# Kernel optimization log

Measured on AMD Instinct MI355X. Metric: run time of the kernel, lower is better.

## Reference

```python
import jax, jax.numpy as jnp
import numpy as np

N_HEADS = 12
EPS = 1e-6
H_DIM = 768


def setup_inputs() -> dict:
    key = jax.random.key(0)
    ks = jax.random.split(key, 10)
    B, M, T, C = 2, 64, 512, H_DIM
    x = jax.random.normal(ks[0], (B, M, T, C), dtype=jnp.float32)
    mask = jnp.ones((B, M, T), dtype=jnp.float32)
    s = 1.0 / np.sqrt(C)
    Wq = jax.random.normal(ks[1], (C, C), dtype=jnp.float32) * s
    bq = jax.random.normal(ks[2], (C,), dtype=jnp.float32) * 0.01
    Wk = jax.random.normal(ks[3], (C, C), dtype=jnp.float32) * s
    bk = jax.random.normal(ks[4], (C,), dtype=jnp.float32) * 0.01
    Wv = jax.random.normal(ks[5], (C, C), dtype=jnp.float32) * s
    bv = jax.random.normal(ks[6], (C,), dtype=jnp.float32) * 0.01
    Wp = jax.random.normal(ks[7], (C, C), dtype=jnp.float32) * s
    bp = jax.random.normal(ks[8], (C,), dtype=jnp.float32) * 0.01
    return {"x": x, "mask": mask, "Wq": Wq, "bq": bq, "Wk": Wk, "bk": bk,
            "Wv": Wv, "bv": bv, "Wp": Wp, "bp": bp}


def reference(x, mask, Wq, bq, Wk, bk, Wv, bv, Wp, bp):
    B, M, T, C = x.shape
    N, D = N_HEADS, C // N_HEADS
    # projections: nn.Linear -> x @ W.T + b, then [B,M,T,N,D] -> [B,M,N,T,D]
    q = (x @ Wq.T + bq).reshape(B, M, T, N, D).transpose(0, 1, 3, 2, 4)
    k = (x @ Wk.T + bk).reshape(B, M, T, N, D).transpose(0, 1, 3, 2, 4)
    v = (x @ Wv.T + bv).reshape(B, M, T, N, D).transpose(0, 1, 3, 2, 4)
    q = jax.nn.elu(q) + 1.0
    k = jax.nn.elu(k) + 1.0
    k = k * mask[:, :, None, :, None]
    # KtV[b,m,n,d,e] = sum_t k[b,m,n,t,d] * v[b,m,n,t,e]   (small [D,D] per head)
    KtV = jnp.einsum('bmntd,bmnte->bmnde', k, v)
    # Z[b,m,n,t] = 1 / (q . sum_t' k + eps)
    Z = 1.0 / (jnp.einsum('bmntd,bmnd->bmnt', q, k.sum(axis=-2)) + EPS)
    # torch code does Z.expand(...,T,D) @ KtV, which equals Z * KtV.sum(over d)
    S = KtV.sum(axis=-2)                       # [B,M,N,E]
    V = Z[..., None] * S[:, :, :, None, :]     # [B,M,N,T,E]
    V = V.transpose(0, 1, 3, 2, 4).reshape(B, M, T, N * D)
    out = V @ Wp.T + bp
    return out
```

## Files before the change

kernel.cpp:

```cpp
#include <hip/hip_runtime.h>
#include <hip/hip_bf16.h>
#include <stdint.h>

typedef short short8 __attribute__((ext_vector_type(8)));
typedef float f32x4 __attribute__((ext_vector_type(4)));

#define EPS_Z 1e-6f

__device__ __forceinline__ unsigned short f2bf(float f) {
  uint32_t b = __float_as_uint(f);
  b += 0x7FFFu + ((b >> 16) & 1u);
  return (unsigned short)(b >> 16);
}
__device__ __forceinline__ float bf2f(unsigned short u) {
  return __uint_as_float(((uint32_t)u) << 16);
}

__device__ __forceinline__ void gl16(const unsigned short* g, unsigned short* l) {
  __builtin_amdgcn_global_load_lds(
      (const __attribute__((address_space(1))) unsigned int*)g,
      (__attribute__((address_space(3))) unsigned int*)l, 16, 0, 0);
}

__global__ __launch_bounds__(256) void k_cvt(const float* __restrict__ in,
                                             unsigned short* __restrict__ out, int n) {
  int i = (blockIdx.x * 256 + threadIdx.x) * 8;
  if (i >= n) return;
  float4 a = *(const float4*)(in + i);
  float4 b = *(const float4*)(in + i + 4);
  union { unsigned short u[8]; short8 v; } r;
  r.u[0] = f2bf(a.x); r.u[1] = f2bf(a.y); r.u[2] = f2bf(a.z); r.u[3] = f2bf(a.w);
  r.u[4] = f2bf(b.x); r.u[5] = f2bf(b.y); r.u[6] = f2bf(b.z); r.u[7] = f2bf(b.w);
  *(short8*)(out + i) = r.v;
}

__global__ __launch_bounds__(512, 2) void k_projqk(
    const unsigned short* __restrict__ xbf,
    const unsigned short* __restrict__ Wkbf,
    const unsigned short* __restrict__ Wqbf,
    const float* __restrict__ bk,
    const float* __restrict__ bq,
    const float* __restrict__ mask,
    float* __restrict__ kd,
    float* __restrict__ ksum_part,
    unsigned short* __restrict__ qbf)
{
  __shared__ unsigned short Ab[128][64];
  __shared__ unsigned short Bkb[128][64];
  __shared__ unsigned short Bqb[128][64];
  __shared__ float rowf[128];
  __shared__ float kcol[2][128];

  const int tid = threadIdx.x;
  const int lane = tid & 63;
  const int wid = tid >> 6;
  const int isQ = wid >> 2;
  const int w2 = wid & 3;
  const int wr = w2 >> 1, wc = w2 & 1;
  const int colTile = blockIdx.x;
  const int rowTile = blockIdx.y;
  const int bm = rowTile >> 2;
  const int trow = rowTile & 3;
  const size_t rowBase = (size_t)rowTile * 128;
  const int colBase = colTile * 128;
  const int lrow = lane & 15;
  const int lgrp = lane >> 4;

  if (tid < 128) rowf[tid] = mask[bm * 512 + trow * 128 + tid];

  f32x4 acc[4][4] = {};

  for (int kt = 0; kt < 12; ++kt) {
    const int k0 = kt * 64;
    __syncthreads();
#pragma unroll
    for (int c = 0; c < 2; ++c) {
      const int chunk = c * 512 + tid;
      const int r = chunk >> 3;
      const int cc = chunk & 7;
      const int scc = cc ^ (r & 7);
      const int ldst = c * 4096 + wid * 512;
      gl16(xbf + (rowBase + r) * 768 + k0 + scc * 8, &Ab[0][0] + ldst);
      gl16(Wkbf + (size_t)(colBase + r) * 768 + k0 + scc * 8, &Bkb[0][0] + ldst);
      gl16(Wqbf + (size_t)(colBase + r) * 768 + k0 + scc * 8, &Bqb[0][0] + ldst);
    }
    __syncthreads();
    const unsigned short* Bsel = isQ ? &Bqb[0][0] : &Bkb[0][0];
#pragma unroll
    for (int kk = 0; kk < 64; kk += 32) {
      short8 av[4], bv4[4];
#pragma unroll
      for (int rf = 0; rf < 4; ++rf) {
        const int row = wr * 64 + rf * 16 + lrow;
        const int cidx = ((kk >> 3) + lgrp) ^ (row & 7);
        av[rf] = *(const short8*)&Ab[row][cidx * 8];
      }
#pragma unroll
      for (int cf = 0; cf < 4; ++cf) {
        const int row = wc * 64 + cf * 16 + lrow;
        const int cidx = ((kk >> 3) + lgrp) ^ (row & 7);
        bv4[cf] = *(const short8*)(Bsel + row * 64 + cidx * 8);
      }
#pragma unroll
      for (int rf = 0; rf < 4; ++rf)
#pragma unroll
        for (int cf = 0; cf < 4; ++cf)
          acc[rf][cf] = __builtin_amdgcn_mfma_f32_16x16x32_bf16(
              av[rf], bv4[cf], acc[rf][cf], 0, 0, 0);
    }
  }

  const float* bias = isQ ? bq : bk;
  float bvv[4];
#pragma unroll
  for (int cf = 0; cf < 4; ++cf)
    bvv[cf] = bias[colBase + wc * 64 + cf * 16 + lrow];
#pragma unroll
  for (int rf = 0; rf < 4; ++rf)
#pragma unroll
    for (int cf = 0; cf < 4; ++cf)
#pragma unroll
      for (int j = 0; j < 4; ++j) {
        float v = acc[rf][cf][j] + bvv[cf];
        v = (v > 0.0f) ? (v + 1.0f) : __expf(v);
        if (!isQ) v *= rowf[wr * 64 + rf * 16 + lgrp * 4 + j];
        acc[rf][cf][j] = v;
      }

  const int head = colTile * 2 + wc;

  if (!isQ) {
#pragma unroll
    for (int rf = 0; rf < 4; ++rf)
#pragma unroll
      for (int j = 0; j < 4; ++j) {
        float s = acc[rf][0][j] + acc[rf][1][j] + acc[rf][2][j] + acc[rf][3][j];
        s += __shfl_xor(s, 1, 64);
        s += __shfl_xor(s, 2, 64);
        s += __shfl_xor(s, 4, 64);
        s += __shfl_xor(s, 8, 64);
        if ((lane & 15) == 0) {
          const int t = trow * 128 + wr * 64 + rf * 16 + lgrp * 4 + j;
          kd[((size_t)bm * 512 + t) * 12 + head] = s;
        }
      }
#pragma unroll
    for (int cf = 0; cf < 4; ++cf) {
      float s = 0.f;
#pragma unroll
      for (int rf = 0; rf < 4; ++rf)
#pragma unroll
        for (int j = 0; j < 4; ++j) s += acc[rf][cf][j];
      s += __shfl_xor(s, 16, 64);
      s += __shfl_xor(s, 32, 64);
      if (lane < 16) kcol[wr][wc * 64 + cf * 16 + lane] = s;
    }
  } else {
#pragma unroll
    for (int rf = 0; rf < 4; ++rf)
#pragma unroll
      for (int j = 0; j < 4; ++j) {
        const int t = trow * 128 + wr * 64 + rf * 16 + lgrp * 4 + j;
        unsigned short* qp = qbf + (((size_t)bm * 12 + head) * 512 + t) * 64 + lrow;
#pragma unroll
        for (int cf = 0; cf < 4; ++cf)
          qp[cf * 16] = f2bf(acc[rf][cf][j]);
      }
  }

  __syncthreads();
  if (tid < 128)
    ksum_part[((size_t)bm * 4 + trow) * 768 + colBase + tid] =
        kcol[0][tid] + kcol[1][tid];
}

__global__ __launch_bounds__(192) void k_xk(const unsigned short* __restrict__ xbf,
                                            const float* __restrict__ kd,
                                            float* __restrict__ xk_part) {
  __shared__ float kdl[128][12];
  const int bm = blockIdx.x, ts = blockIdx.y, tid = threadIdx.x;
  for (int i = tid; i < 128 * 12; i += 192)
    kdl[i / 12][i % 12] = kd[((size_t)bm * 512 + ts * 128 + i / 12) * 12 + (i % 12)];
  __syncthreads();
  float a[12][4];
#pragma unroll
  for (int n = 0; n < 12; ++n)
#pragma unroll
    for (int j = 0; j < 4; ++j) a[n][j] = 0.f;
  const int c = tid * 4;
  const unsigned short* xp = xbf + ((size_t)bm * 512 + ts * 128) * 768 + c;
  for (int t = 0; t < 128; ++t) {
    ushort4 xv = *(const ushort4*)(xp + (size_t)t * 768);
    const float x0 = bf2f(xv.x), x1 = bf2f(xv.y), x2 = bf2f(xv.z), x3 = bf2f(xv.w);
#pragma unroll
    for (int n = 0; n < 12; ++n) {
      const float kv = kdl[t][n];
      a[n][0] += kv * x0; a[n][1] += kv * x1; a[n][2] += kv * x2; a[n][3] += kv * x3;
    }
  }
  float* op = xk_part + ((size_t)bm * 4 + ts) * 12 * 768 + c;
#pragma unroll
  for (int n = 0; n < 12; ++n)
    *(float4*)(op + (size_t)n * 768) = make_float4(a[n][0], a[n][1], a[n][2], a[n][3]);
}

__global__ __launch_bounds__(256) void k_sg(const float* __restrict__ ksum_part,
                                            const float* __restrict__ xk_part,
                                            const float* __restrict__ Wv,
                                            const float* __restrict__ bv,
                                            const float* __restrict__ Wp,
                                            float* __restrict__ G) {
  __shared__ __align__(16) float xk_l[768];
  __shared__ __align__(16) float S_l[64];
  __shared__ float kdsum_s;
  const int bm = blockIdx.x, n = blockIdx.y, tid = threadIdx.x;

  if (tid < 192) {
    const float* xp = xk_part + (size_t)bm * 4 * 9216 + n * 768 + tid * 4;
    float4 a = *(const float4*)(xp);
    float4 b = *(const float4*)(xp + 9216);
    float4 c = *(const float4*)(xp + 18432);
    float4 d = *(const float4*)(xp + 27648);
    *(float4*)&xk_l[tid * 4] = make_float4(a.x + b.x + c.x + d.x,
                                           a.y + b.y + c.y + d.y,
                                           a.z + b.z + c.z + d.z,
                                           a.w + b.w + c.w + d.w);
  } else {
    const int d = tid - 192;
    const float* kp = ksum_part + (size_t)bm * 4 * 768 + n * 64 + d;
    float s = kp[0] + kp[768] + kp[1536] + kp[2304];
    s += __shfl_xor(s, 1, 64);
    s += __shfl_xor(s, 2, 64);
    s += __shfl_xor(s, 4, 64);
    s += __shfl_xor(s, 8, 64);
    s += __shfl_xor(s, 16, 64);
    s += __shfl_xor(s, 32, 64);
    if (d == 0) kdsum_s = s;
  }
  __syncthreads();

  {
    const int e = tid >> 2, q = tid & 3;
    const float4* wv = (const float4*)(Wv + (size_t)(n * 64 + e) * 768 + q * 192);
    const float4* xp4 = (const float4*)(xk_l + q * 192);
    float s = 0.f;
#pragma unroll
    for (int i = 0; i < 48; ++i) {
      float4 w = wv[i], xx = xp4[i];
      s += w.x * xx.x + w.y * xx.y + w.z * xx.z + w.w * xx.w;
    }
    s += __shfl_xor(s, 1, 64);
    s += __shfl_xor(s, 2, 64);
    if (q == 0) S_l[e] = s + bv[n * 64 + e] * kdsum_s;
  }
  __syncthreads();

#pragma unroll
  for (int r = 0; r < 3; ++r) {
    const int p = r * 256 + tid;
    const float4* wp = (const float4*)(Wp + (size_t)p * 768 + n * 64);
    const float4* sp = (const float4*)S_l;
    float g = 0.f;
#pragma unroll
    for (int i = 0; i < 16; ++i) {
      float4 w = wp[i], s = sp[i];
      g += w.x * s.x + w.y * s.y + w.z * s.z + w.w * s.w;
    }
    G[((size_t)bm * 12 + n) * 768 + p] = g;
  }
}

__global__ __launch_bounds__(256) void k_z(const unsigned short* __restrict__ qbf,
                                           const float* __restrict__ ksum_part,
                                           float* __restrict__ Z) {
  __shared__ float ksum_l[768];
  const int bm = blockIdx.x, ts = blockIdx.y, tid = threadIdx.x;
  for (int i = tid; i < 768; i += 256) {
    const float* kp = ksum_part + (size_t)bm * 3072 + i;
    ksum_l[i] = kp[0] + kp[768] + kp[1536] + kp[2304];
  }
  __syncthreads();
#pragma unroll
  for (int i = 0; i < 6; ++i) {
    const int task = i * 256 + tid;
    const int n = task >> 7;
    const int t = ts * 128 + (task & 127);
    const unsigned short* qp = qbf + (((size_t)bm * 12 + n) * 512 + t) * 64;
    const float* kp = &ksum_l[n * 64];
    float s = 0.f;
#pragma unroll
    for (int c = 0; c < 8; ++c) {
      short8 qv = *(const short8*)(qp + c * 8);
      s += bf2f((unsigned short)qv[0]) * kp[c * 8 + 0]
         + bf2f((unsigned short)qv[1]) * kp[c * 8 + 1]
         + bf2f((unsigned short)qv[2]) * kp[c * 8 + 2]
         + bf2f((unsigned short)qv[3]) * kp[c * 8 + 3]
         + bf2f((unsigned short)qv[4]) * kp[c * 8 + 4]
         + bf2f((unsigned short)qv[5]) * kp[c * 8 + 5]
         + bf2f((unsigned short)qv[6]) * kp[c * 8 + 6]
         + bf2f((unsigned short)qv[7]) * kp[c * 8 + 7];
    }
    Z[((size_t)bm * 12 + n) * 512 + t] = 1.0f / (s + EPS_Z);
  }
}

__global__ __launch_bounds__(256) void k_out(const float* __restrict__ Z,
                                             const float* __restrict__ G,
                                             const float* __restrict__ bp,
                                             float* __restrict__ outp) {
  __shared__ __align__(16) float G_l[9216];
  __shared__ float Z_l[768];
  __shared__ __align__(16) float bp_l[768];
  const int bm = blockIdx.x;
  const int tbase = blockIdx.y * 64;
  const int tid = threadIdx.x;
  for (int i = tid; i < 9216; i += 256) G_l[i] = G[(size_t)bm * 9216 + i];
  for (int i = tid; i < 768; i += 256) {
    bp_l[i] = bp[i];
    Z_l[i] = Z[((size_t)bm * 12 + (i >> 6)) * 512 + tbase + (i & 63)];
  }
  __syncthreads();
  for (int it = 0; it < 48; ++it) {
    const int idx = it * 1024 + tid * 4;
    const int t = idx / 768;
    const int p = idx - t * 768;
    float4 o = *(const float4*)&bp_l[p];
#pragma unroll
    for (int n = 0; n < 12; ++n) {
      const float z = Z_l[n * 64 + t];
      const float4 g = *(const float4*)&G_l[n * 768 + p];
      o.x += z * g.x; o.y += z * g.y; o.z += z * g.z; o.w += z * g.w;
    }
    *(float4*)&outp[((size_t)bm * 512 + tbase + t) * 768 + p] = o;
  }
}

extern "C" void kernel_launch(void* const* d_in, const int* in_sizes, int n_in,
                              void* d_out, int out_size, void* d_ws, size_t ws_size,
                              hipStream_t stream) {
  const float* x    = (const float*)d_in[0];
  const float* mask = (const float*)d_in[1];
  const float* Wq   = (const float*)d_in[2];
  const float* bq   = (const float*)d_in[3];
  const float* Wk   = (const float*)d_in[4];
  const float* bk   = (const float*)d_in[5];
  const float* Wv   = (const float*)d_in[6];
  const float* bv   = (const float*)d_in[7];
  const float* Wp   = (const float*)d_in[8];
  const float* bp   = (const float*)d_in[9];
  float* outp = (float*)d_out;

  char* ws = (char*)d_ws;
  unsigned short* xbf  = (unsigned short*)(ws);
  unsigned short* Wkbf = (unsigned short*)(ws + 100663296);
  unsigned short* Wqbf = (unsigned short*)(ws + 101842944);
  float* kd        = (float*)(ws + 103022592);
  float* ksum_part = (float*)(ws + 106168320);
  float* xk_part   = (float*)(ws + 107741184);
  float* Zb        = (float*)(ws + 126615552);
  float* G         = (float*)(ws + 129761280);
  unsigned short* qbf = (unsigned short*)d_out;

  hipLaunchKernelGGL(k_cvt, dim3(24576), dim3(256), 0, stream, x, xbf, 50331648);
  hipLaunchKernelGGL(k_cvt, dim3(288), dim3(256), 0, stream, Wk, Wkbf, 589824);
  hipLaunchKernelGGL(k_cvt, dim3(288), dim3(256), 0, stream, Wq, Wqbf, 589824);
  hipLaunchKernelGGL(k_projqk, dim3(6, 512), dim3(512), 0, stream,
                     xbf, Wkbf, Wqbf, bk, bq, mask, kd, ksum_part, qbf);
  hipLaunchKernelGGL(k_xk, dim3(128, 4), dim3(192), 0, stream, xbf, kd, xk_part);
  hipLaunchKernelGGL(k_sg, dim3(128, 12), dim3(256), 0, stream,
                     ksum_part, xk_part, Wv, bv, Wp, G);
  hipLaunchKernelGGL(k_z, dim3(128, 4), dim3(256), 0, stream, qbf, ksum_part, Zb);
  hipLaunchKernelGGL(k_out, dim3(128, 8), dim3(256), 0, stream, Zb, G, bp, outp);
}
```

Baseline: 494.2 us.

## Merge conversion launches, compute K and Q per wave, swizzle grid, fuse xk and Z kernels

The three bf16 conversion launches become one kernel, and the xk and Z kernels are merged into one launch that branches on block index. The QK projection now uses 4 waves per block, and each wave computes both the K and Q accumulators from the same A fragments. This halves the A-fragment LDS reads per output, but each wave now holds twice the accumulators, which raises register pressure. A flat grid with a row-tile swizzle is added to improve L2 locality, and the changes together also aim to cut launch overhead.

```diff
diff --git a/kernel.cpp b/kernel.cpp
--- a/kernel.cpp
+++ b/kernel.cpp
@@ -22,10 +22,18 @@
       (__attribute__((address_space(3))) unsigned int*)l, 16, 0, 0);
 }
 
-__global__ __launch_bounds__(256) void k_cvt(const float* __restrict__ in,
-                                             unsigned short* __restrict__ out, int n) {
-  int i = (blockIdx.x * 256 + threadIdx.x) * 8;
-  if (i >= n) return;
+__global__ __launch_bounds__(256) void k_cvt_all(
+    const float* __restrict__ x, const float* __restrict__ Wk,
+    const float* __restrict__ Wq, unsigned short* __restrict__ xbf,
+    unsigned short* __restrict__ Wkbf, unsigned short* __restrict__ Wqbf) {
+  const int bid = blockIdx.x;
+  const float* in;
+  unsigned short* out;
+  int base;
+  if (bid < 24576)      { in = x;  out = xbf;  base = bid; }
+  else if (bid < 24864) { in = Wk; out = Wkbf; base = bid - 24576; }
+  else                  { in = Wq; out = Wqbf; base = bid - 24864; }
+  const int i = (base * 256 + threadIdx.x) * 8;
   float4 a = *(const float4*)(in + i);
   float4 b = *(const float4*)(in + i + 4);
   union { unsigned short u[8]; short8 v; } r;
@@ -34,7 +42,7 @@
   *(short8*)(out + i) = r.v;
 }
 
-__global__ __launch_bounds__(512, 2) void k_projqk(
+__global__ __launch_bounds__(256, 2) void k_projqk(
     const unsigned short* __restrict__ xbf,
     const unsigned short* __restrict__ Wkbf,
     const unsigned short* __restrict__ Wqbf,
@@ -54,11 +62,11 @@
   const int tid = threadIdx.x;
   const int lane = tid & 63;
   const int wid = tid >> 6;
-  const int isQ = wid >> 2;
-  const int w2 = wid & 3;
-  const int wr = w2 >> 1, wc = w2 & 1;
-  const int colTile = blockIdx.x;
-  const int rowTile = blockIdx.y;
+  const int wr = wid >> 1, wc = wid & 1;
+  const int flat = blockIdx.x;
+  const int swz = (flat & 7) * 384 + (flat >> 3);
+  const int colTile = swz % 6;
+  const int rowTile = swz / 6;
   const int bm = rowTile >> 2;
   const int trow = rowTile & 3;
   const size_t rowBase = (size_t)rowTile * 128;
@@ -68,27 +76,27 @@
 
   if (tid < 128) rowf[tid] = mask[bm * 512 + trow * 128 + tid];
 
-  f32x4 acc[4][4] = {};
+  f32x4 ak[4][4] = {};
+  f32x4 aq[4][4] = {};
 
   for (int kt = 0; kt < 12; ++kt) {
     const int k0 = kt * 64;
     __syncthreads();
 #pragma unroll
-    for (int c = 0; c < 2; ++c) {
-      const int chunk = c * 512 + tid;
+    for (int c = 0; c < 4; ++c) {
+      const int chunk = c * 256 + tid;
       const int r = chunk >> 3;
       const int cc = chunk & 7;
       const int scc = cc ^ (r & 7);
-      const int ldst = c * 4096 + wid * 512;
+      const int ldst = c * 2048 + wid * 512;
       gl16(xbf + (rowBase + r) * 768 + k0 + scc * 8, &Ab[0][0] + ldst);
       gl16(Wkbf + (size_t)(colBase + r) * 768 + k0 + scc * 8, &Bkb[0][0] + ldst);
       gl16(Wqbf + (size_t)(colBase + r) * 768 + k0 + scc * 8, &Bqb[0][0] + ldst);
     }
     __syncthreads();
-    const unsigned short* Bsel = isQ ? &Bqb[0][0] : &Bkb[0][0];
 #pragma unroll
     for (int kk = 0; kk < 64; kk += 32) {
-      short8 av[4], bv4[4];
+      short8 av[4], bvk[4], bvq[4];
 #pragma unroll
       for (int rf = 0; rf < 4; ++rf) {
         const int row = wr * 64 + rf * 16 + lrow;
@@ -99,74 +107,79 @@
       for (int cf = 0; cf < 4; ++cf) {
         const int row = wc * 64 + cf * 16 + lrow;
         const int cidx = ((kk >> 3) + lgrp) ^ (row & 7);
-        bv4[cf] = *(const short8*)(Bsel + row * 64 + cidx * 8);
+        bvk[cf] = *(const short8*)&Bkb[row][cidx * 8];
+        bvq[cf] = *(const short8*)&Bqb[row][cidx * 8];
       }
 #pragma unroll
       for (int rf = 0; rf < 4; ++rf)
 #pragma unroll
-        for (int cf = 0; cf < 4; ++cf)
-          acc[rf][cf] = __builtin_amdgcn_mfma_f32_16x16x32_bf16(
-              av[rf], bv4[cf], acc[rf][cf], 0, 0, 0);
-    }
-  }
-
-  const float* bias = isQ ? bq : bk;
-  float bvv[4];
-#pragma unroll
-  for (int cf = 0; cf < 4; ++cf)
-    bvv[cf] = bias[colBase + wc * 64 + cf * 16 + lrow];
+        for (int cf = 0; cf < 4; ++cf) {
+          ak[rf][cf] = __builtin_amdgcn_mfma_f32_16x16x32_bf16(
+              av[rf], bvk[cf], ak[rf][cf], 0, 0, 0);
+          aq[rf][cf] = __builtin_amdgcn_mfma_f32_16x16x32_bf16(
+              av[rf], bvq[cf], aq[rf][cf], 0, 0, 0);
+        }
+    }
+  }
+
+  float bkv[4], bqv[4];
+#pragma unroll
+  for (int cf = 0; cf < 4; ++cf) {
+    bkv[cf] = bk[colBase + wc * 64 + cf * 16 + lrow];
+    bqv[cf] = bq[colBase + wc * 64 + cf * 16 + lrow];
+  }
 #pragma unroll
   for (int rf = 0; rf < 4; ++rf)
 #pragma unroll
     for (int cf = 0; cf < 4; ++cf)
 #pragma unroll
       for (int j = 0; j < 4; ++j) {
-        float v = acc[rf][cf][j] + bvv[cf];
+        float v = ak[rf][cf][j] + bkv[cf];
         v = (v > 0.0f) ? (v + 1.0f) : __expf(v);
-        if (!isQ) v *= rowf[wr * 64 + rf * 16 + lgrp * 4 + j];
-        acc[rf][cf][j] = v;
+        ak[rf][cf][j] = v * rowf[wr * 64 + rf * 16 + lgrp * 4 + j];
+        float u = aq[rf][cf][j] + bqv[cf];
+        aq[rf][cf][j] = (u > 0.0f) ? (u + 1.0f) : __expf(u);
       }
 
   const int head = colTile * 2 + wc;
 
-  if (!isQ) {
+#pragma unroll
+  for (int rf = 0; rf < 4; ++rf)
+#pragma unroll
+    for (int j = 0; j < 4; ++j) {
+      float s = ak[rf][0][j] + ak[rf][1][j] + ak[rf][2][j] + ak[rf][3][j];
+      s += __shfl_xor(s, 1, 64);
+      s += __shfl_xor(s, 2, 64);
+      s += __shfl_xor(s, 4, 64);
+      s += __shfl_xor(s, 8, 64);
+      if ((lane & 15) == 0) {
+        const int t = trow * 128 + wr * 64 + rf * 16 + lgrp * 4 + j;
+        kd[((size_t)bm * 512 + t) * 12 + head] = s;
+      }
+    }
+
+#pragma unroll
+  for (int cf = 0; cf < 4; ++cf) {
+    float s = 0.f;
 #pragma unroll
     for (int rf = 0; rf < 4; ++rf)
 #pragma unroll
-      for (int j = 0; j < 4; ++j) {
-        float s = acc[rf][0][j] + acc[rf][1][j] + acc[rf][2][j] + acc[rf][3][j];
-        s += __shfl_xor(s, 1, 64);
-        s += __shfl_xor(s, 2, 64);
-        s += __shfl_xor(s, 4, 64);
-        s += __shfl_xor(s, 8, 64);
-        if ((lane & 15) == 0) {
-          const int t = trow * 128 + wr * 64 + rf * 16 + lgrp * 4 + j;
-          kd[((size_t)bm * 512 + t) * 12 + head] = s;
-        }
-      }
-#pragma unroll
-    for (int cf = 0; cf < 4; ++cf) {
-      float s = 0.f;
-#pragma unroll
-      for (int rf = 0; rf < 4; ++rf)
-#pragma unroll
-        for (int j = 0; j < 4; ++j) s += acc[rf][cf][j];
-      s += __shfl_xor(s, 16, 64);
-      s += __shfl_xor(s, 32, 64);
-      if (lane < 16) kcol[wr][wc * 64 + cf * 16 + lane] = s;
-    }
-  } else {
-#pragma unroll
-    for (int rf = 0; rf < 4; ++rf)
-#pragma unroll
-      for (int j = 0; j < 4; ++j) {
-        const int t = trow * 128 + wr * 64 + rf * 16 + lgrp * 4 + j;
-        unsigned short* qp = qbf + (((size_t)bm * 12 + head) * 512 + t) * 64 + lrow;
-#pragma unroll
-        for (int cf = 0; cf < 4; ++cf)
-          qp[cf * 16] = f2bf(acc[rf][cf][j]);
-      }
-  }
+      for (int j = 0; j < 4; ++j) s += ak[rf][cf][j];
+    s += __shfl_xor(s, 16, 64);
+    s += __shfl_xor(s, 32, 64);
+    if (lane < 16) kcol[wr][wc * 64 + cf * 16 + lane] = s;
+  }
+
+#pragma unroll
+  for (int rf = 0; rf < 4; ++rf)
+#pragma unroll
+    for (int j = 0; j < 4; ++j) {
+      const int t = trow * 128 + wr * 64 + rf * 16 + lgrp * 4 + j;
+      unsigned short* qp = qbf + (((size_t)bm * 12 + head) * 512 + t) * 64 + lrow;
+#pragma unroll
+      for (int cf = 0; cf < 4; ++cf)
+        qp[cf * 16] = f2bf(aq[rf][cf][j]);
+    }
 
   __syncthreads();
   if (tid < 128)
@@ -174,34 +187,73 @@
         kcol[0][tid] + kcol[1][tid];
 }
 
-__global__ __launch_bounds__(192) void k_xk(const unsigned short* __restrict__ xbf,
-                                            const float* __restrict__ kd,
-                                            float* __restrict__ xk_part) {
-  __shared__ float kdl[128][12];
-  const int bm = blockIdx.x, ts = blockIdx.y, tid = threadIdx.x;
-  for (int i = tid; i < 128 * 12; i += 192)
-    kdl[i / 12][i % 12] = kd[((size_t)bm * 512 + ts * 128 + i / 12) * 12 + (i % 12)];
-  __syncthreads();
-  float a[12][4];
-#pragma unroll
-  for (int n = 0; n < 12; ++n)
-#pragma unroll
-    for (int j = 0; j < 4; ++j) a[n][j] = 0.f;
-  const int c = tid * 4;
-  const unsigned short* xp = xbf + ((size_t)bm * 512 + ts * 128) * 768 + c;
-  for (int t = 0; t < 128; ++t) {
-    ushort4 xv = *(const ushort4*)(xp + (size_t)t * 768);
-    const float x0 = bf2f(xv.x), x1 = bf2f(xv.y), x2 = bf2f(xv.z), x3 = bf2f(xv.w);
-#pragma unroll
-    for (int n = 0; n < 12; ++n) {
-      const float kv = kdl[t][n];
-      a[n][0] += kv * x0; a[n][1] += kv * x1; a[n][2] += kv * x2; a[n][3] += kv * x3;
-    }
-  }
-  float* op = xk_part + ((size_t)bm * 4 + ts) * 12 * 768 + c;
-#pragma unroll
-  for (int n = 0; n < 12; ++n)
-    *(float4*)(op + (size_t)n * 768) = make_float4(a[n][0], a[n][1], a[n][2], a[n][3]);
+__global__ __launch_bounds__(256) void k_xkz(const unsigned short* __restrict__ xbf,
+                                             const float* __restrict__ kd,
+                                             float* __restrict__ xk_part,
+                                             const unsigned short* __restrict__ qbf,
+                                             const float* __restrict__ ksum_part,
+                                             float* __restrict__ Z) {
+  const int bid = blockIdx.x, tid = threadIdx.x;
+  if (bid < 512) {
+    __shared__ float kdl[128][12];
+    const int bm = bid >> 2, ts = bid & 3;
+    for (int i = tid; i < 128 * 12; i += 256)
+      kdl[i / 12][i % 12] = kd[((size_t)bm * 512 + ts * 128 + i / 12) * 12 + (i % 12)];
+    __syncthreads();
+    if (tid < 192) {
+      float a[12][4];
+#pragma unroll
+      for (int n = 0; n < 12; ++n)
+#pragma unroll
+        for (int j = 0; j < 4; ++j) a[n][j] = 0.f;
+      const int c = tid * 4;
+      const unsigned short* xp = xbf + ((size_t)bm * 512 + ts * 128) * 768 + c;
+      for (int t = 0; t < 128; ++t) {
+        ushort4 xv = *(const ushort4*)(xp + (size_t)t * 768);
+        const float x0 = bf2f(xv.x), x1 = bf2f(xv.y), x2 = bf2f(xv.z), x3 = bf2f(xv.w);
+#pragma unroll
+        for (int n = 0; n < 12; ++n) {
+          const float kv = kdl[t][n];
+          a[n][0] += kv * x0; a[n][1] += kv * x1; a[n][2] += kv * x2; a[n][3] += kv * x3;
+        }
+      }
+      float* op = xk_part + ((size_t)bm * 4 + ts) * 12 * 768 + c;
+#pragma unroll
+      for (int n = 0; n < 12; ++n)
+        *(float4*)(op + (size_t)n * 768) = make_float4(a[n][0], a[n][1], a[n][2], a[n][3]);
+    }
+  } else {
+    __shared__ float ksum_l[768];
+    const int b2 = bid - 512;
+    const int bm = b2 >> 2, ts = b2 & 3;
+    for (int i = tid; i < 768; i += 256) {
+      const float* kp = ksum_part + (size_t)bm * 3072 + i;
+      ksum_l[i] = kp[0] + kp[768] + kp[1536] + kp[2304];
+    }
+    __syncthreads();
+#pragma unroll
+    for (int i = 0; i < 6; ++i) {
+      const int task = i * 256 + tid;
+      const int n = task >> 7;
+      const int t = ts * 128 + (task & 127);
+      const unsigned short* qp = qbf + (((size_t)bm * 12 + n) * 512 + t) * 64;
+      const float* kp = &ksum_l[n * 64];
+      float s = 0.f;
+#pragma unroll
+      for (int c = 0; c < 8; ++c) {
+        short8 qv = *(const short8*)(qp + c * 8);
+        s += bf2f((unsigned short)qv[0]) * kp[c * 8 + 0]
+           + bf2f((unsigned short)qv[1]) * kp[c * 8 + 1]
+           + bf2f((unsigned short)qv[2]) * kp[c * 8 + 2]
+           + bf2f((unsigned short)qv[3]) * kp[c * 8 + 3]
+           + bf2f((unsigned short)qv[4]) * kp[c * 8 + 4]
+           + bf2f((unsigned short)qv[5]) * kp[c * 8 + 5]
+           + bf2f((unsigned short)qv[6]) * kp[c * 8 + 6]
+           + bf2f((unsigned short)qv[7]) * kp[c * 8 + 7];
+      }
+      Z[((size_t)bm * 12 + n) * 512 + t] = 1.0f / (s + EPS_Z);
+    }
+  }
 }
 
 __global__ __launch_bounds__(256) void k_sg(const float* __restrict__ ksum_part,
@@ -270,40 +322,6 @@
   }
 }
 
-__global__ __launch_bounds__(256) void k_z(const unsigned short* __restrict__ qbf,
-                                           const float* __restrict__ ksum_part,
-                                           float* __restrict__ Z) {
-  __shared__ float ksum_l[768];
-  const int bm = blockIdx.x, ts = blockIdx.y, tid = threadIdx.x;
-  for (int i = tid; i < 768; i += 256) {
-    const float* kp = ksum_part + (size_t)bm * 3072 + i;
-    ksum_l[i] = kp[0] + kp[768] + kp[1536] + kp[2304];
-  }
-  __syncthreads();
-#pragma unroll
-  for (int i = 0; i < 6; ++i) {
-    const int task = i * 256 + tid;
-    const int n = task >> 7;
-    const int t = ts * 128 + (task & 127);
-    const unsigned short* qp = qbf + (((size_t)bm * 12 + n) * 512 + t) * 64;
-    const float* kp = &ksum_l[n * 64];
-    float s = 0.f;
-#pragma unroll
-    for (int c = 0; c < 8; ++c) {
-      short8 qv = *(const short8*)(qp + c * 8);
-      s += bf2f((unsigned short)qv[0]) * kp[c * 8 + 0]
-         + bf2f((unsigned short)qv[1]) * kp[c * 8 + 1]
-         + bf2f((unsigned short)qv[2]) * kp[c * 8 + 2]
-         + bf2f((unsigned short)qv[3]) * kp[c * 8 + 3]
-         + bf2f((unsigned short)qv[4]) * kp[c * 8 + 4]
-         + bf2f((unsigned short)qv[5]) * kp[c * 8 + 5]
-         + bf2f((unsigned short)qv[6]) * kp[c * 8 + 6]
-         + bf2f((unsigned short)qv[7]) * kp[c * 8 + 7];
-    }
-    Z[((size_t)bm * 12 + n) * 512 + t] = 1.0f / (s + EPS_Z);
-  }
-}
-
 __global__ __launch_bounds__(256) void k_out(const float* __restrict__ Z,
                                              const float* __restrict__ G,
                                              const float* __restrict__ bp,
@@ -361,14 +379,13 @@
   float* G         = (float*)(ws + 129761280);
   unsigned short* qbf = (unsigned short*)d_out;
 
-  hipLaunchKernelGGL(k_cvt, dim3(24576), dim3(256), 0, stream, x, xbf, 50331648);
-  hipLaunchKernelGGL(k_cvt, dim3(288), dim3(256), 0, stream, Wk, Wkbf, 589824);
-  hipLaunchKernelGGL(k_cvt, dim3(288), dim3(256), 0, stream, Wq, Wqbf, 589824);
-  hipLaunchKernelGGL(k_projqk, dim3(6, 512), dim3(512), 0, stream,
+  hipLaunchKernelGGL(k_cvt_all, dim3(25152), dim3(256), 0, stream,
+                     x, Wk, Wq, xbf, Wkbf, Wqbf);
+  hipLaunchKernelGGL(k_projqk, dim3(3072), dim3(256), 0, stream,
                      xbf, Wkbf, Wqbf, bk, bq, mask, kd, ksum_part, qbf);
-  hipLaunchKernelGGL(k_xk, dim3(128, 4), dim3(192), 0, stream, xbf, kd, xk_part);
+  hipLaunchKernelGGL(k_xkz, dim3(1024), dim3(256), 0, stream,
+                     xbf, kd, xk_part, qbf, ksum_part, Zb);
   hipLaunchKernelGGL(k_sg, dim3(128, 12), dim3(256), 0, stream,
                      ksum_part, xk_part, Wv, bv, Wp, G);
-  hipLaunchKernelGGL(k_z, dim3(128, 4), dim3(256), 0, stream, qbf, ksum_part, Zb);
   hipLaunchKernelGGL(k_out, dim3(128, 8), dim3(256), 0, stream, Zb, G, bp, outp);
 }
```

Measured after the change: 482.1 us. 1.03x faster.
